# Kernel optimization log

Hardware: AMD Instinct MI355X
Metric: run time of the kernel (lower is better)

## Reference

```python
import jax, jax.numpy as jnp
import numpy as np

TOKENS, H, I = 2048, 3584, 18944


def setup_inputs() -> dict:
    key = jax.random.key(0)
    ks = jax.random.split(key, 8)
    x = jax.random.normal(ks[0], (TOKENS, H), dtype=jnp.float32)
    gate_w = jax.random.randint(ks[1], (I, H), -127, 128, dtype=jnp.int32).astype(jnp.int8)
    up_w = jax.random.randint(ks[2], (I, H), -127, 128, dtype=jnp.int32).astype(jnp.int8)
    down_w = jax.random.randint(ks[3], (H, I), -127, 128, dtype=jnp.int32).astype(jnp.int8)
    # realistic small per-tensor scales
    gate_w_scale = jnp.float32(0.01) * (jnp.float32(0.5) + jax.random.uniform(ks[4], ()))
    up_w_scale = jnp.float32(0.01) * (jnp.float32(0.5) + jax.random.uniform(ks[5], ()))
    down_w_scale = jnp.float32(0.01) * (jnp.float32(0.5) + jax.random.uniform(ks[6], ()))
    down_input_scale = jnp.float32(0.05) * (jnp.float32(0.5) + jax.random.uniform(ks[7], ()))
    return {"x": x, "gate_w": gate_w, "up_w": up_w, "down_w": down_w,
            "gate_w_scale": gate_w_scale, "up_w_scale": up_w_scale,
            "down_w_scale": down_w_scale, "down_input_scale": down_input_scale}


def _quant_per_token(x):
    # dynamic per-token symmetric int8 quantization
    s = jnp.max(jnp.abs(x), axis=-1, keepdims=True) / jnp.float32(127.0)
    s = jnp.maximum(s, jnp.float32(1e-8))
    q = jnp.clip(jnp.round(x / s), -127, 127).astype(jnp.int8)
    return q, s  # q: [T, K] int8, s: [T, 1] fp32


def _int8_gemm(q, w):
    # q: [T, K] int8, w: [N, K] int8 -> [T, N] int32 accumulate
    return jax.lax.dot(q, w.T, preferred_element_type=jnp.int32)


def reference(x, gate_w, up_w, down_w, gate_w_scale, up_w_scale,
              down_w_scale, down_input_scale):
    # fc1 (gate & up): per-token dynamic activation quant, shared quantized input
    qx, sx = _quant_per_token(x)
    gate = _int8_gemm(qx, gate_w).astype(jnp.float32) * sx * gate_w_scale  # [T, I]
    up = _int8_gemm(qx, up_w).astype(jnp.float32) * sx * up_w_scale        # [T, I]
    h = jax.nn.silu(gate) * up  # SwiGLU, fp32
    # fc2 (down): static per-tensor activation quant with stored input scale
    qh = jnp.clip(jnp.round(h / down_input_scale), -127, 127).astype(jnp.int8)
    out = _int8_gemm(qh, down_w).astype(jnp.float32) * (down_input_scale * down_w_scale)
    return out  # [T, H] fp32
```

## Files before the change

### kernel.cpp

```cpp
#include <hip/hip_runtime.h>
#include <stdint.h>

#define TOKENS 2048
#define H_DIM 3584
#define I_DIM 18944

typedef int v4i __attribute__((ext_vector_type(4)));

__device__ __forceinline__ void async_copy16(const void* g, void* lds) {
    __builtin_amdgcn_global_load_lds(
        (const __attribute__((address_space(1))) void*)g,
        (__attribute__((address_space(3))) void*)lds,
        16, 0, 0);
}


__global__ __launch_bounds__(256)
void pack3_kernel(const int* __restrict__ s0, int8_t* __restrict__ d0,
                  const int* __restrict__ s1, int8_t* __restrict__ d1,
                  const int* __restrict__ s2, int8_t* __restrict__ d2,
                  int pb) {
    int b = blockIdx.x;
    const int* src; int8_t* dst;
    if (b >= 2 * pb)    { src = s2; dst = d2; b -= 2 * pb; }
    else if (b >= pb)   { src = s1; dst = d1; b -= pb; }
    else                { src = s0; dst = d0; }
    const int i = b * 256 + threadIdx.x;
    v4i w = ((const v4i*)src)[i];
    int packed = (w.x & 0xff) | ((w.y & 0xff) << 8) |
                 ((w.z & 0xff) << 16) | (w.w << 24);
    ((int*)dst)[i] = packed;
}

__global__ __launch_bounds__(256)
void quant_x_kernel(const float* __restrict__ x,
                    int8_t* __restrict__ qx,
                    float* __restrict__ sx) {
    const int row = blockIdx.x;
    const float4* xr = (const float4*)(x + (size_t)row * H_DIM);
    float m = 0.0f;
    for (int j = threadIdx.x; j < 896; j += 256) {
        float4 v = xr[j];
        m = fmaxf(m, fmaxf(fmaxf(fabsf(v.x), fabsf(v.y)),
                           fmaxf(fabsf(v.z), fabsf(v.w))));
    }
    for (int off = 32; off > 0; off >>= 1)
        m = fmaxf(m, __shfl_down(m, off, 64));
    __shared__ float wmax[4];
    if ((threadIdx.x & 63) == 0) wmax[threadIdx.x >> 6] = m;
    __syncthreads();
    float mm = fmaxf(fmaxf(wmax[0], wmax[1]), fmaxf(wmax[2], wmax[3]));
    float s = fmaxf(mm / 127.0f, 1e-8f);
    if (threadIdx.x == 0) sx[row] = s;
    int* qrow = (int*)(qx + (size_t)row * H_DIM);
    for (int j = threadIdx.x; j < 896; j += 256) {
        float4 v = xr[j];
        int q0 = (int)fminf(fmaxf(rintf(v.x / s), -127.0f), 127.0f);
        int q1 = (int)fminf(fmaxf(rintf(v.y / s), -127.0f), 127.0f);
        int q2 = (int)fminf(fmaxf(rintf(v.z / s), -127.0f), 127.0f);
        int q3 = (int)fminf(fmaxf(rintf(v.w / s), -127.0f), 127.0f);
        qrow[j] = (q0 & 0xff) | ((q1 & 0xff) << 8) | ((q2 & 0xff) << 16) |
                  (q3 << 24);
    }
}

#define FC1_LOADA(MH) do { _Pragma("unroll")                                   \
  for (int m_ = 0; m_ < 4; ++m_) {                                             \
    a[m_][0] = *(const v4i*)(Ab + aOff + (MH)*8192 + m_*2048 + sw0);           \
    a[m_][1] = *(const v4i*)(Ab + aOff + (MH)*8192 + m_*2048 + sw1);           \
  } } while (0)

#define FC1_LOADB(NF) do {                                                     \
    bg[NF][0] = *(const v4i*)(Bb + bOff + (NF)*2048 + sw0);                    \
    bg[NF][1] = *(const v4i*)(Bb + bOff + (NF)*2048 + sw1);                    \
    bu[NF][0] = *(const v4i*)(Bb + 16384 + bOff + (NF)*2048 + sw0);            \
    bu[NF][1] = *(const v4i*)(Bb + 16384 + bOff + (NF)*2048 + sw1);            \
  } while (0)

#define FC1_MFMA(MH, NF) do { _Pragma("unroll")                                \
  for (int m_ = 0; m_ < 4; ++m_) {                                             \
    accG[(MH)*4+m_][NF] = __builtin_amdgcn_mfma_i32_16x16x64_i8(               \
        a[m_][0], bg[NF][0], accG[(MH)*4+m_][NF], 0, 0, 0);                    \
    accU[(MH)*4+m_][NF] = __builtin_amdgcn_mfma_i32_16x16x64_i8(               \
        a[m_][0], bu[NF][0], accU[(MH)*4+m_][NF], 0, 0, 0);                    \
    accG[(MH)*4+m_][NF] = __builtin_amdgcn_mfma_i32_16x16x64_i8(               \
        a[m_][1], bg[NF][1], accG[(MH)*4+m_][NF], 0, 0, 0);                    \
    accU[(MH)*4+m_][NF] = __builtin_amdgcn_mfma_i32_16x16x64_i8(               \
        a[m_][1], bu[NF][1], accU[(MH)*4+m_][NF], 0, 0, 0);                    \
  } } while (0)

__global__ __launch_bounds__(512, 2)
void fc1_kernel(const int8_t* __restrict__ qx,
                const float* __restrict__ sx,
                const int8_t* __restrict__ gw,
                const int8_t* __restrict__ uw,
                const float* __restrict__ gws,
                const float* __restrict__ uws,
                const float* __restrict__ dis,
                int8_t* __restrict__ qh) {
    __shared__ __align__(16) int8_t lds[2][65536];

    const int tid  = threadIdx.x;
    const int wave = tid >> 6;
    const int lane = tid & 63;
    const int wr = wave >> 2;
    const int wc = wave & 3;
    const int fr = lane & 15;
    const int fq = lane >> 4;

    const int bid = blockIdx.x;
    const int gid = (bid & 7) * 148 + (bid >> 3);
    const int m0 = (gid & 7) * 256;
    const int n0 = (gid >> 3) * 128;

    const int rowS  = tid >> 3;
    const int kOffS = ((tid & 7) ^ (rowS & 7)) * 16;
    const int8_t* gA = qx + (size_t)(m0 + rowS) * H_DIM + kOffS;
    const int8_t* gG = gw + (size_t)(n0 + rowS) * H_DIM + kOffS;
    const int8_t* gU = uw + (size_t)(n0 + rowS) * H_DIM + kOffS;

    const int sw0 = (fq ^ (fr & 7)) * 16;
    const int sw1 = ((4 + fq) ^ (fr & 7)) * 16;
    const int aOff = (wr * 128 + fr) * 128;
    const int bOff = (wc * 32 + fr) * 128;

    v4i accG[8][2] = {};
    v4i accU[8][2] = {};
    v4i a[4][2], bg[2][2], bu[2][2];

    {
        int8_t* lA = &lds[0][tid * 16];
        int8_t* lB = &lds[0][32768 + tid * 16];
#pragma unroll
        for (int j = 0; j < 4; ++j)
            async_copy16(gA + (size_t)(64 * j) * H_DIM, lA + j * 8192);
        async_copy16(gG,                         lB);
        async_copy16(gG + (size_t)64 * H_DIM,    lB + 8192);
        async_copy16(gU,                         lB + 16384);
        async_copy16(gU + (size_t)64 * H_DIM,    lB + 24576);
    }
    __syncthreads();

    for (int kt = 0; kt < H_DIM / 128; ++kt) {
        const int8_t* Ab = lds[kt & 1];
        const int8_t* Bb = Ab + 32768;
        int8_t* An = (int8_t*)lds[(kt & 1) ^ 1];
        int8_t* Bn = An + 32768;
        const bool pf = (kt + 1) < (H_DIM / 128);
        const int  kN = (kt + 1) * 128;

        if (pf) {
            int8_t* lA = An + tid * 16;
#pragma unroll
            for (int j = 0; j < 4; ++j)
                async_copy16(gA + kN + (size_t)(64 * j) * H_DIM, lA + j * 8192);
        }
        FC1_LOADA(0);
        FC1_LOADB(0);
        __builtin_amdgcn_s_barrier();
        __builtin_amdgcn_s_setprio(1);
        FC1_MFMA(0, 0);
        __builtin_amdgcn_s_setprio(0);
        __builtin_amdgcn_s_barrier();

        if (pf) {
            int8_t* lB = Bn + tid * 16;
            async_copy16(gG + kN,                      lB);
            async_copy16(gG + kN + (size_t)64 * H_DIM, lB + 8192);
            async_copy16(gU + kN,                      lB + 16384);
            async_copy16(gU + kN + (size_t)64 * H_DIM, lB + 24576);
        }
        FC1_LOADB(1);
        __builtin_amdgcn_s_barrier();
        __builtin_amdgcn_s_setprio(1);
        FC1_MFMA(0, 1);
        __builtin_amdgcn_s_setprio(0);
        __builtin_amdgcn_s_barrier();

        FC1_LOADA(1);
        __builtin_amdgcn_s_barrier();
        __builtin_amdgcn_s_setprio(1);
        FC1_MFMA(1, 0);
        __builtin_amdgcn_s_setprio(0);
        __builtin_amdgcn_s_barrier();

        __builtin_amdgcn_s_setprio(1);
        FC1_MFMA(1, 1);
        __builtin_amdgcn_s_setprio(0);
        __syncthreads();
    }

    const float gscale = *gws;
    const float uscale = *uws;
    const float dis_v  = *dis;

#pragma unroll
    for (int M = 0; M < 8; ++M) {
#pragma unroll
        for (int r = 0; r < 4; ++r) {
            const int row = m0 + wr * 128 + M * 16 + fq * 4 + r;
            const float s  = sx[row];
            const float gs = s * gscale;
            const float us = s * uscale;
            const size_t base = (size_t)row * I_DIM + n0 + wc * 32;
#pragma unroll
            for (int nf = 0; nf < 2; ++nf) {
                float g = (float)accG[M][nf][r] * gs;
                float u = (float)accU[M][nf][r] * us;
                float h = (g / (1.0f + expf(-g))) * u;
                float q = rintf(h / dis_v);
                q = fminf(fmaxf(q, -127.0f), 127.0f);
                qh[base + nf * 16 + fr] = (int8_t)q;
            }
        }
    }
}

#define FC2_LOADA() do { _Pragma("unroll")                                     \
  for (int m_ = 0; m_ < 4; ++m_) {                                             \
    a[m_][0] = *(const v4i*)(Ab + aOff + m_*2048 + sw0);                       \
    a[m_][1] = *(const v4i*)(Ab + aOff + m_*2048 + sw1);                       \
  } } while (0)

#define FC2_LOADB(NH) do { _Pragma("unroll")                                   \
  for (int n_ = 0; n_ < 2; ++n_) {                                             \
    b[n_][0] = *(const v4i*)(Bb + bOff + ((NH)*2+n_)*2048 + sw0);              \
    b[n_][1] = *(const v4i*)(Bb + bOff + ((NH)*2+n_)*2048 + sw1);              \
  } } while (0)

#define FC2_MFMA(NH) do { _Pragma("unroll")                                    \
  for (int m_ = 0; m_ < 4; ++m_) { _Pragma("unroll")                           \
    for (int n_ = 0; n_ < 2; ++n_) {                                           \
      acc[m_][(NH)*2+n_] = __builtin_amdgcn_mfma_i32_16x16x64_i8(              \
          a[m_][0], b[n_][0], acc[m_][(NH)*2+n_], 0, 0, 0);                    \
      acc[m_][(NH)*2+n_] = __builtin_amdgcn_mfma_i32_16x16x64_i8(              \
          a[m_][1], b[n_][1], acc[m_][(NH)*2+n_], 0, 0, 0);                    \
    } } } while (0)

__global__ __launch_bounds__(256, 2)
void fc2_kernel(const int8_t* __restrict__ qh,
                const int8_t* __restrict__ dw,
                const float* __restrict__ dws,
                const float* __restrict__ dis,
                float* __restrict__ out) {
    __shared__ __align__(16) int8_t lds[2][32768];

    const int tid  = threadIdx.x;
    const int wave = tid >> 6;
    const int lane = tid & 63;
    const int wr = wave >> 1;
    const int wc = wave & 1;
    const int fr = lane & 15;
    const int fq = lane >> 4;

    const int bid = blockIdx.x;
    const int gid = (bid & 7) * 56 + (bid >> 3);
    const int m0 = (gid & 15) * 128;
    const int n0 = (gid >> 4) * 128;

    const int rowS  = tid >> 3;
    const int kOffS = ((tid & 7) ^ (rowS & 7)) * 16;
    const int8_t* gA = qh + (size_t)(m0 + rowS) * I_DIM + kOffS;
    const int8_t* gW = dw + (size_t)(n0 + rowS) * I_DIM + kOffS;

    const int sw0 = (fq ^ (fr & 7)) * 16;
    const int sw1 = ((4 + fq) ^ (fr & 7)) * 16;
    const int aOff = (wr * 64 + fr) * 128;
    const int bOff = (wc * 64 + fr) * 128;

    v4i acc[4][4] = {};
    v4i a[4][2], b[2][2];

    {
        int8_t* lA = &lds[0][tid * 16];
        int8_t* lB = &lds[0][16384 + tid * 16];
#pragma unroll
        for (int j = 0; j < 4; ++j) {
            async_copy16(gA + (size_t)(32 * j) * I_DIM, lA + j * 4096);
            async_copy16(gW + (size_t)(32 * j) * I_DIM, lB + j * 4096);
        }
    }
    __syncthreads();

    for (int kt = 0; kt < I_DIM / 128; ++kt) {
        const int8_t* Ab = lds[kt & 1];
        const int8_t* Bb = Ab + 16384;
        int8_t* An = (int8_t*)lds[(kt & 1) ^ 1];
        int8_t* Bn = An + 16384;
        const bool pf = (kt + 1) < (I_DIM / 128);
        const int  kN = (kt + 1) * 128;

        if (pf) {
            int8_t* lA = An + tid * 16;
            int8_t* lB = Bn + tid * 16;
#pragma unroll
            for (int j = 0; j < 4; ++j) {
                async_copy16(gA + kN + (size_t)(32 * j) * I_DIM, lA + j * 4096);
                async_copy16(gW + kN + (size_t)(32 * j) * I_DIM, lB + j * 4096);
            }
        }
        FC2_LOADA();
        FC2_LOADB(0);
        __builtin_amdgcn_s_barrier();
        __builtin_amdgcn_s_setprio(1);
        FC2_MFMA(0);
        __builtin_amdgcn_s_setprio(0);
        __builtin_amdgcn_s_barrier();

        FC2_LOADB(1);
        __builtin_amdgcn_s_barrier();
        __builtin_amdgcn_s_setprio(1);
        FC2_MFMA(1);
        __builtin_amdgcn_s_setprio(0);
        __syncthreads();
    }

    const float sc = (*dis) * (*dws);
#pragma unroll
    for (int m_ = 0; m_ < 4; ++m_)
#pragma unroll
        for (int n_ = 0; n_ < 4; ++n_)
#pragma unroll
            for (int r = 0; r < 4; ++r) {
                const int row = m0 + wr * 64 + m_ * 16 + fq * 4 + r;
                const int col = n0 + wc * 64 + n_ * 16 + fr;
                out[(size_t)row * H_DIM + col] = (float)acc[m_][n_][r] * sc;
            }
}

extern "C" void kernel_launch(void* const* d_in, const int* in_sizes, int n_in,
                              void* d_out, int out_size, void* d_ws, size_t ws_size,
                              hipStream_t stream) {
    const float* x    = (const float*)d_in[0];
    const int*   gw32 = (const int*)d_in[1];
    const int*   uw32 = (const int*)d_in[2];
    const int*   dw32 = (const int*)d_in[3];
    const float* gws  = (const float*)d_in[4];
    const float* uws  = (const float*)d_in[5];
    const float* dws  = (const float*)d_in[6];
    const float* dis  = (const float*)d_in[7];
    float* out = (float*)d_out;

    const size_t W = (size_t)I_DIM * H_DIM;
    int8_t* qx  = (int8_t*)d_ws;
    float*  sx  = (float*)((char*)d_ws + (size_t)TOKENS * H_DIM);
    int8_t* qh  = (int8_t*)((char*)d_ws + (size_t)TOKENS * H_DIM + TOKENS * 4);
    int8_t* gw8 = (int8_t*)((char*)d_ws + (size_t)TOKENS * H_DIM + TOKENS * 4
                            + (size_t)TOKENS * I_DIM);
    int8_t* uw8 = gw8 + W;
    int8_t* dw8 = uw8 + W;

    const int pb = (int)(W / 4 / 256);
    pack3_kernel<<<3 * pb, 256, 0, stream>>>(gw32, gw8, uw32, uw8, dw32, dw8, pb);

    quant_x_kernel<<<TOKENS, 256, 0, stream>>>(x, qx, sx);

    fc1_kernel<<<(TOKENS / 256) * (I_DIM / 128), 512, 0, stream>>>(
        qx, sx, gw8, uw8, gws, uws, dis, qh);

    fc2_kernel<<<(TOKENS / 128) * (H_DIM / 128), 256, 0, stream>>>(
        qh, dw8, dws, dis, out);
}
```

Baseline: 1.157 ms.

## Use 4-stage K=64 async LDS pipeline in fc1/fc2 and widen weight packing

Both GEMM kernels move from a double-buffered K=128 tile to a four-slot ring of K=64 tiles. Loads run three stages ahead, and explicit vmcnt waits plus one barrier per step replace the full syncthreads. The LDS layout and swizzle are rebuilt for 64-byte rows, and the MFMA inner loop uses a single A/B fragment per step. The pack kernel also has each thread handle 16 elements with vector stores, so far fewer blocks are launched. The risks are a fragile hand-written waitcnt scheme and more barrier rounds per unit of K.

```diff
diff --git a/kernel.cpp b/kernel.cpp
--- a/kernel.cpp
+++ b/kernel.cpp
@@ -25,11 +25,15 @@
     if (b >= 2 * pb)    { src = s2; dst = d2; b -= 2 * pb; }
     else if (b >= pb)   { src = s1; dst = d1; b -= pb; }
     else                { src = s0; dst = d0; }
-    const int i = b * 256 + threadIdx.x;
-    v4i w = ((const v4i*)src)[i];
-    int packed = (w.x & 0xff) | ((w.y & 0xff) << 8) |
-                 ((w.z & 0xff) << 16) | (w.w << 24);
-    ((int*)dst)[i] = packed;
+    const size_t i = (size_t)b * 256 + threadIdx.x;
+    const v4i* s = (const v4i*)src + i * 4;
+    v4i w0 = s[0], w1 = s[1], w2 = s[2], w3 = s[3];
+    v4i p;
+    p.x = (w0.x & 0xff) | ((w0.y & 0xff) << 8) | ((w0.z & 0xff) << 16) | (w0.w << 24);
+    p.y = (w1.x & 0xff) | ((w1.y & 0xff) << 8) | ((w1.z & 0xff) << 16) | (w1.w << 24);
+    p.z = (w2.x & 0xff) | ((w2.y & 0xff) << 8) | ((w2.z & 0xff) << 16) | (w2.w << 24);
+    p.w = (w3.x & 0xff) | ((w3.y & 0xff) << 8) | ((w3.z & 0xff) << 16) | (w3.w << 24);
+    ((v4i*)dst)[i] = p;
 }
 
 __global__ __launch_bounds__(256)
@@ -64,30 +68,37 @@
     }
 }
 
-#define FC1_LOADA(MH) do { _Pragma("unroll")                                   \
-  for (int m_ = 0; m_ < 4; ++m_) {                                             \
-    a[m_][0] = *(const v4i*)(Ab + aOff + (MH)*8192 + m_*2048 + sw0);           \
-    a[m_][1] = *(const v4i*)(Ab + aOff + (MH)*8192 + m_*2048 + sw1);           \
+#define FC1_STAGE_A(PS, KQ) do {                                               \
+    int8_t* _lA = &lds[PS][0] + tid * 16;                                      \
+    async_copy16(gA + (size_t)(KQ) * 64,                      _lA);            \
+    async_copy16(gA + (size_t)(KQ) * 64 + 128 * H_DIM,        _lA + 8192);     \
+  } while (0)
+
+#define FC1_STAGE_B(PS, KQ) do {                                               \
+    int8_t* _lB = &lds[PS][16384] + tid * 16;                                  \
+    async_copy16(gG + (size_t)(KQ) * 64, _lB);                                 \
+    async_copy16(gU + (size_t)(KQ) * 64, _lB + 8192);                          \
+  } while (0)
+
+#define FC1_READ_A(MH) do { _Pragma("unroll")                                  \
+  for (int m_ = 0; m_ < 4; ++m_)                                               \
+    a[m_] = *(const v4i*)(Ab + aOff + (MH) * 4096 + m_ * 1024);                \
+  } while (0)
+
+#define FC1_READ_B() do { _Pragma("unroll")                                    \
+  for (int n_ = 0; n_ < 2; ++n_) {                                             \
+    bg[n_] = *(const v4i*)(Bb + bOff + n_ * 1024);                             \
+    bu[n_] = *(const v4i*)(Bb + bOff + 8192 + n_ * 1024);                      \
   } } while (0)
 
-#define FC1_LOADB(NF) do {                                                     \
-    bg[NF][0] = *(const v4i*)(Bb + bOff + (NF)*2048 + sw0);                    \
-    bg[NF][1] = *(const v4i*)(Bb + bOff + (NF)*2048 + sw1);                    \
-    bu[NF][0] = *(const v4i*)(Bb + 16384 + bOff + (NF)*2048 + sw0);            \
-    bu[NF][1] = *(const v4i*)(Bb + 16384 + bOff + (NF)*2048 + sw1);            \
-  } while (0)
-
-#define FC1_MFMA(MH, NF) do { _Pragma("unroll")                                \
-  for (int m_ = 0; m_ < 4; ++m_) {                                             \
-    accG[(MH)*4+m_][NF] = __builtin_amdgcn_mfma_i32_16x16x64_i8(               \
-        a[m_][0], bg[NF][0], accG[(MH)*4+m_][NF], 0, 0, 0);                    \
-    accU[(MH)*4+m_][NF] = __builtin_amdgcn_mfma_i32_16x16x64_i8(               \
-        a[m_][0], bu[NF][0], accU[(MH)*4+m_][NF], 0, 0, 0);                    \
-    accG[(MH)*4+m_][NF] = __builtin_amdgcn_mfma_i32_16x16x64_i8(               \
-        a[m_][1], bg[NF][1], accG[(MH)*4+m_][NF], 0, 0, 0);                    \
-    accU[(MH)*4+m_][NF] = __builtin_amdgcn_mfma_i32_16x16x64_i8(               \
-        a[m_][1], bu[NF][1], accU[(MH)*4+m_][NF], 0, 0, 0);                    \
-  } } while (0)
+#define FC1_MFMA16(MH) do { _Pragma("unroll")                                  \
+  for (int m_ = 0; m_ < 4; ++m_) { _Pragma("unroll")                           \
+    for (int n_ = 0; n_ < 2; ++n_) {                                           \
+      accG[(MH)*4+m_][n_] = __builtin_amdgcn_mfma_i32_16x16x64_i8(             \
+          a[m_], bg[n_], accG[(MH)*4+m_][n_], 0, 0, 0);                        \
+      accU[(MH)*4+m_][n_] = __builtin_amdgcn_mfma_i32_16x16x64_i8(             \
+          a[m_], bu[n_], accU[(MH)*4+m_][n_], 0, 0, 0);                        \
+    } } } while (0)
 
 __global__ __launch_bounds__(512, 2)
 void fc1_kernel(const int8_t* __restrict__ qx,
@@ -98,7 +109,7 @@
                 const float* __restrict__ uws,
                 const float* __restrict__ dis,
                 int8_t* __restrict__ qh) {
-    __shared__ __align__(16) int8_t lds[2][65536];
+    __shared__ __align__(16) int8_t lds[4][32768];
 
     const int tid  = threadIdx.x;
     const int wave = tid >> 6;
@@ -113,81 +124,60 @@
     const int m0 = (gid & 7) * 256;
     const int n0 = (gid >> 3) * 128;
 
-    const int rowS  = tid >> 3;
-    const int kOffS = ((tid & 7) ^ (rowS & 7)) * 16;
+    const int rowS  = tid >> 2;
+    const int kOffS = ((tid & 3) ^ ((tid >> 3) & 3)) * 16;
     const int8_t* gA = qx + (size_t)(m0 + rowS) * H_DIM + kOffS;
     const int8_t* gG = gw + (size_t)(n0 + rowS) * H_DIM + kOffS;
     const int8_t* gU = uw + (size_t)(n0 + rowS) * H_DIM + kOffS;
 
-    const int sw0 = (fq ^ (fr & 7)) * 16;
-    const int sw1 = ((4 + fq) ^ (fr & 7)) * 16;
-    const int aOff = (wr * 128 + fr) * 128;
-    const int bOff = (wc * 32 + fr) * 128;
+    const int swz  = (fq ^ ((fr >> 1) & 3)) * 16;
+    const int aOff = wr * 8192 + fr * 64 + swz;
+    const int bOff = wc * 2048 + fr * 64 + swz;
 
     v4i accG[8][2] = {};
     v4i accU[8][2] = {};
-    v4i a[4][2], bg[2][2], bu[2][2];
-
-    {
-        int8_t* lA = &lds[0][tid * 16];
-        int8_t* lB = &lds[0][32768 + tid * 16];
-#pragma unroll
-        for (int j = 0; j < 4; ++j)
-            async_copy16(gA + (size_t)(64 * j) * H_DIM, lA + j * 8192);
-        async_copy16(gG,                         lB);
-        async_copy16(gG + (size_t)64 * H_DIM,    lB + 8192);
-        async_copy16(gU,                         lB + 16384);
-        async_copy16(gU + (size_t)64 * H_DIM,    lB + 24576);
-    }
-    __syncthreads();
-
-    for (int kt = 0; kt < H_DIM / 128; ++kt) {
-        const int8_t* Ab = lds[kt & 1];
-        const int8_t* Bb = Ab + 32768;
-        int8_t* An = (int8_t*)lds[(kt & 1) ^ 1];
-        int8_t* Bn = An + 32768;
-        const bool pf = (kt + 1) < (H_DIM / 128);
-        const int  kN = (kt + 1) * 128;
-
-        if (pf) {
-            int8_t* lA = An + tid * 16;
-#pragma unroll
-            for (int j = 0; j < 4; ++j)
-                async_copy16(gA + kN + (size_t)(64 * j) * H_DIM, lA + j * 8192);
-        }
-        FC1_LOADA(0);
-        FC1_LOADB(0);
+    v4i a[4], bg[2], bu[2];
+
+    const int NT = H_DIM / 64;
+    FC1_STAGE_A(0, 0); FC1_STAGE_B(0, 0);
+    FC1_STAGE_A(1, 1); FC1_STAGE_B(1, 1);
+    FC1_STAGE_A(2, 2); FC1_STAGE_B(2, 2);
+    __builtin_amdgcn_sched_barrier(0);
+    asm volatile("s_waitcnt vmcnt(8)" ::: "memory");
+    __builtin_amdgcn_s_barrier();
+    __builtin_amdgcn_sched_barrier(0);
+
+    for (int q = 0; q < NT; ++q) {
+        const int rs = q & 3;
+        const int ps = (q + 3) & 3;
+        const bool pf = (q + 3) < NT;
+        const int8_t* Ab = &lds[rs][0];
+        const int8_t* Bb = &lds[rs][16384];
+
+        if (pf) FC1_STAGE_A(ps, q + 3);
+        FC1_READ_A(0);
+        FC1_READ_B();
         __builtin_amdgcn_s_barrier();
         __builtin_amdgcn_s_setprio(1);
-        FC1_MFMA(0, 0);
+        FC1_MFMA16(0);
         __builtin_amdgcn_s_setprio(0);
         __builtin_amdgcn_s_barrier();
-
-        if (pf) {
-            int8_t* lB = Bn + tid * 16;
-            async_copy16(gG + kN,                      lB);
-            async_copy16(gG + kN + (size_t)64 * H_DIM, lB + 8192);
-            async_copy16(gU + kN,                      lB + 16384);
-            async_copy16(gU + kN + (size_t)64 * H_DIM, lB + 24576);
-        }
-        FC1_LOADB(1);
+        __builtin_amdgcn_sched_barrier(0);
+
+        if (pf) FC1_STAGE_B(ps, q + 3);
+        FC1_READ_A(1);
         __builtin_amdgcn_s_barrier();
         __builtin_amdgcn_s_setprio(1);
-        FC1_MFMA(0, 1);
+        FC1_MFMA16(1);
         __builtin_amdgcn_s_setprio(0);
-        __builtin_amdgcn_s_barrier();
-
-        FC1_LOADA(1);
-        __builtin_amdgcn_s_barrier();
-        __builtin_amdgcn_s_setprio(1);
-        FC1_MFMA(1, 0);
-        __builtin_amdgcn_s_setprio(0);
-        __builtin_amdgcn_s_barrier();
-
-        __builtin_amdgcn_s_setprio(1);
-        FC1_MFMA(1, 1);
-        __builtin_amdgcn_s_setprio(0);
-        __syncthreads();
+        __builtin_amdgcn_sched_barrier(0);
+        if (q < NT - 3)       asm volatile("s_waitcnt vmcnt(8)" ::: "memory");
+        else if (q == NT - 3) asm volatile("s_waitcnt vmcnt(4)" ::: "memory");
+        else if (q == NT - 2) asm volatile("s_waitcnt vmcnt(0)" ::: "memory");
+        if (q < NT - 1) {
+            __builtin_amdgcn_s_barrier();
+            __builtin_amdgcn_sched_barrier(0);
+        }
     }
 
     const float gscale = *gws;
@@ -216,26 +206,29 @@
     }
 }
 
-#define FC2_LOADA() do { _Pragma("unroll")                                     \
-  for (int m_ = 0; m_ < 4; ++m_) {                                             \
-    a[m_][0] = *(const v4i*)(Ab + aOff + m_*2048 + sw0);                       \
-    a[m_][1] = *(const v4i*)(Ab + aOff + m_*2048 + sw1);                       \
+#define FC2_STAGE(PS, KQ) do {                                                 \
+    int8_t* _lA = &lds[PS][0]    + tid * 16;                                   \
+    int8_t* _lB = &lds[PS][8192] + tid * 16;                                   \
+    async_copy16(gA + (size_t)(KQ) * 64,                  _lA);                \
+    async_copy16(gA + (size_t)(KQ) * 64 + 64 * I_DIM,     _lA + 4096);         \
+    async_copy16(gW + (size_t)(KQ) * 64,                  _lB);                 \
+    async_copy16(gW + (size_t)(KQ) * 64 + 64 * I_DIM,     _lB + 4096);         \
+  } while (0)
+
+#define FC2_READ() do { _Pragma("unroll")                                      \
+  for (int m_ = 0; m_ < 4; ++m_)                                               \
+    a[m_] = *(const v4i*)(Ab + aOff + m_ * 1024);                              \
+  _Pragma("unroll")                                                            \
+  for (int n_ = 0; n_ < 4; ++n_)                                               \
+    b[n_] = *(const v4i*)(Ab + bOff + n_ * 1024);                              \
+  } while (0)
+
+#define FC2_MFMA16() do { _Pragma("unroll")                                    \
+  for (int m_ = 0; m_ < 4; ++m_) { _Pragma("unroll")                           \
+    for (int n_ = 0; n_ < 4; ++n_)                                             \
+      acc[m_][n_] = __builtin_amdgcn_mfma_i32_16x16x64_i8(                     \
+          a[m_], b[n_], acc[m_][n_], 0, 0, 0);                                 \
   } } while (0)
-
-#define FC2_LOADB(NH) do { _Pragma("unroll")                                   \
-  for (int n_ = 0; n_ < 2; ++n_) {                                             \
-    b[n_][0] = *(const v4i*)(Bb + bOff + ((NH)*2+n_)*2048 + sw0);              \
-    b[n_][1] = *(const v4i*)(Bb + bOff + ((NH)*2+n_)*2048 + sw1);              \
-  } } while (0)
-
-#define FC2_MFMA(NH) do { _Pragma("unroll")                                    \
-  for (int m_ = 0; m_ < 4; ++m_) { _Pragma("unroll")                           \
-    for (int n_ = 0; n_ < 2; ++n_) {                                           \
-      acc[m_][(NH)*2+n_] = __builtin_amdgcn_mfma_i32_16x16x64_i8(              \
-          a[m_][0], b[n_][0], acc[m_][(NH)*2+n_], 0, 0, 0);                    \
-      acc[m_][(NH)*2+n_] = __builtin_amdgcn_mfma_i32_16x16x64_i8(              \
-          a[m_][1], b[n_][1], acc[m_][(NH)*2+n_], 0, 0, 0);                    \
-    } } } while (0)
 
 __global__ __launch_bounds__(256, 2)
 void fc2_kernel(const int8_t* __restrict__ qh,
@@ -243,7 +236,7 @@
                 const float* __restrict__ dws,
                 const float* __restrict__ dis,
                 float* __restrict__ out) {
-    __shared__ __align__(16) int8_t lds[2][32768];
+    __shared__ __align__(16) int8_t lds[4][16384];
 
     const int tid  = threadIdx.x;
     const int wave = tid >> 6;
@@ -258,61 +251,47 @@
     const int m0 = (gid & 15) * 128;
     const int n0 = (gid >> 4) * 128;
 
-    const int rowS  = tid >> 3;
-    const int kOffS = ((tid & 7) ^ (rowS & 7)) * 16;
+    const int rowS  = tid >> 2;
+    const int kOffS = ((tid & 3) ^ ((tid >> 3) & 3)) * 16;
     const int8_t* gA = qh + (size_t)(m0 + rowS) * I_DIM + kOffS;
     const int8_t* gW = dw + (size_t)(n0 + rowS) * I_DIM + kOffS;
 
-    const int sw0 = (fq ^ (fr & 7)) * 16;
-    const int sw1 = ((4 + fq) ^ (fr & 7)) * 16;
-    const int aOff = (wr * 64 + fr) * 128;
-    const int bOff = (wc * 64 + fr) * 128;
+    const int swz  = (fq ^ ((fr >> 1) & 3)) * 16;
+    const int aOff = wr * 4096 + fr * 64 + swz;
+    const int bOff = 8192 + wc * 4096 + fr * 64 + swz;
 
     v4i acc[4][4] = {};
-    v4i a[4][2], b[2][2];
-
-    {
-        int8_t* lA = &lds[0][tid * 16];
-        int8_t* lB = &lds[0][16384 + tid * 16];
-#pragma unroll
-        for (int j = 0; j < 4; ++j) {
-            async_copy16(gA + (size_t)(32 * j) * I_DIM, lA + j * 4096);
-            async_copy16(gW + (size_t)(32 * j) * I_DIM, lB + j * 4096);
-        }
-    }
-    __syncthreads();
-
-    for (int kt = 0; kt < I_DIM / 128; ++kt) {
-        const int8_t* Ab = lds[kt & 1];
-        const int8_t* Bb = Ab + 16384;
-        int8_t* An = (int8_t*)lds[(kt & 1) ^ 1];
-        int8_t* Bn = An + 16384;
-        const bool pf = (kt + 1) < (I_DIM / 128);
-        const int  kN = (kt + 1) * 128;
-
-        if (pf) {
-            int8_t* lA = An + tid * 16;
-            int8_t* lB = Bn + tid * 16;
-#pragma unroll
-            for (int j = 0; j < 4; ++j) {
-                async_copy16(gA + kN + (size_t)(32 * j) * I_DIM, lA + j * 4096);
-                async_copy16(gW + kN + (size_t)(32 * j) * I_DIM, lB + j * 4096);
-            }
-        }
-        FC2_LOADA();
-        FC2_LOADB(0);
+    v4i a[4], b[4];
+
+    const int NT = I_DIM / 64;
+    FC2_STAGE(0, 0);
+    FC2_STAGE(1, 1);
+    FC2_STAGE(2, 2);
+    __builtin_amdgcn_sched_barrier(0);
+    asm volatile("s_waitcnt vmcnt(8)" ::: "memory");
+    __builtin_amdgcn_s_barrier();
+    __builtin_amdgcn_sched_barrier(0);
+
+    for (int q = 0; q < NT; ++q) {
+        const int rs = q & 3;
+        const int ps = (q + 3) & 3;
+        const bool pf = (q + 3) < NT;
+        const int8_t* Ab = &lds[rs][0];
+
+        if (pf) FC2_STAGE(ps, q + 3);
+        FC2_READ();
         __builtin_amdgcn_s_barrier();
         __builtin_amdgcn_s_setprio(1);
-        FC2_MFMA(0);
+        FC2_MFMA16();
         __builtin_amdgcn_s_setprio(0);
-        __builtin_amdgcn_s_barrier();
-
-        FC2_LOADB(1);
-        __builtin_amdgcn_s_barrier();
-        __builtin_amdgcn_s_setprio(1);
-        FC2_MFMA(1);
-        __builtin_amdgcn_s_setprio(0);
-        __syncthreads();
+        __builtin_amdgcn_sched_barrier(0);
+        if (q < NT - 3)       asm volatile("s_waitcnt vmcnt(8)" ::: "memory");
+        else if (q == NT - 3) asm volatile("s_waitcnt vmcnt(4)" ::: "memory");
+        else if (q == NT - 2) asm volatile("s_waitcnt vmcnt(0)" ::: "memory");
+        if (q < NT - 1) {
+            __builtin_amdgcn_s_barrier();
+            __builtin_amdgcn_sched_barrier(0);
+        }
     }
 
     const float sc = (*dis) * (*dws);
@@ -350,7 +329,7 @@
     int8_t* uw8 = gw8 + W;
     int8_t* dw8 = uw8 + W;
 
-    const int pb = (int)(W / 4 / 256);
+    const int pb = (int)(W / 16 / 256);
     pack3_kernel<<<3 * pb, 256, 0, stream>>>(gw32, gw8, uw32, uw8, dw32, dw8, pb);
 
     quant_x_kernel<<<TOKENS, 256, 0, stream>>>(x, qx, sx);
```

Measured after the change: 1.228 ms. +6.2%, slower.
